# Performance work log

Hardware: AMD Instinct MI355X
Metric: run time of the kernel (lower is better)

The kernel has to match this reference:

```python
import jax, jax.numpy as jnp
import numpy as np

B, C, H, W = 16, 256, 64, 64
NH, HD, NM = 4, 32, 4  # heads, head_dim, memory tokens
HID = NH * HD


def rms_norm(x, g):
    # F.normalize(x, dim=1) * sqrt(C) * g  (channel dim = 1)
    norm = jnp.maximum(jnp.linalg.norm(x, axis=1, keepdims=True), 1e-12)
    return x / norm * (x.shape[1] ** 0.5) * g


def setup_inputs() -> dict:
    key = jax.random.key(0)
    ks = jax.random.split(key, 5)
    return {
        "x": jax.random.normal(ks[0], (B, C, H, W), jnp.float32),
        "g_in": jnp.ones((1, C, 1, 1), jnp.float32),
        "mem_kv": jax.random.normal(ks[1], (2, NH, HD, NM), jnp.float32),
        "w_qkv": jax.random.normal(ks[2], (HID * 3, C), jnp.float32) * (C ** -0.5),
        "w_out": jax.random.normal(ks[3], (C, HID), jnp.float32) * (HID ** -0.5),
        "b_out": jnp.zeros((C,), jnp.float32),
        "g_out": jnp.ones((1, C, 1, 1), jnp.float32),
    }


def reference(x, g_in, mem_kv, w_qkv, w_out, b_out, g_out):
    b, c, h, w = x.shape
    n = h * w
    scale = HD ** -0.5

    xn = rms_norm(x, g_in)
    # 1x1 conv as matmul over channel dim: [B, 3*HID, H, W]
    qkv = jnp.einsum('oc,bchw->bohw', w_qkv, xn)
    q, k, v = jnp.split(qkv, 3, axis=1)
    # b (h d) x y -> b h d n
    q = q.reshape(b, NH, HD, n)
    k = k.reshape(b, NH, HD, n)
    v = v.reshape(b, NH, HD, n)

    # prepend memory key/value tokens: [b, h, d, NM + n]
    mk = jnp.broadcast_to(mem_kv[0], (b, NH, HD, NM))
    mv = jnp.broadcast_to(mem_kv[1], (b, NH, HD, NM))
    k = jnp.concatenate([mk, k], axis=-1)
    v = jnp.concatenate([mv, v], axis=-1)

    q = jax.nn.softmax(q, axis=-2) * scale  # softmax over head_dim
    k = jax.nn.softmax(k, axis=-1)          # softmax over tokens

    context = jnp.einsum('bhdn,bhen->bhde', k, v)  # [b, h, d, e]
    out = jnp.einsum('bhde,bhdn->bhen', context, q)  # [b, h, e, n]
    out = out.reshape(b, HID, h, w)

    out = jnp.einsum('oc,bchw->bohw', w_out, out) + b_out[None, :, None, None]
    return rms_norm(out, g_out)
```

## Files before the change

kernel.cpp:

```cpp
#include <hip/hip_runtime.h>
#include <math.h>

typedef unsigned short u16;
typedef unsigned int u32;

#define NBATCH 16
#define NCH    256
#define NPIX   4096
#define NHEAD  4
#define HDIM   32
#define NMEM   4
#define HID    128
#define OC3    384
#define SCALE_Q 0.17677669529663687f

typedef __bf16 bf16x8 __attribute__((ext_vector_type(8)));
typedef float  f32x4  __attribute__((ext_vector_type(4)));

__device__ __forceinline__ float bf2f(u16 u){ return __uint_as_float(((u32)u)<<16); }
__device__ __forceinline__ u16 f2bf(float f){
  u32 x = __float_as_uint(f);
  x += 0x7fffu + ((x>>16)&1u);
  return (u16)(x>>16);
}
__device__ __forceinline__ void unpack8(int4 v, float* o){
  u32 a=(u32)v.x, b=(u32)v.y, c=(u32)v.z, d=(u32)v.w;
  o[0]=__uint_as_float(a<<16); o[1]=__uint_as_float(a&0xffff0000u);
  o[2]=__uint_as_float(b<<16); o[3]=__uint_as_float(b&0xffff0000u);
  o[4]=__uint_as_float(c<<16); o[5]=__uint_as_float(c&0xffff0000u);
  o[6]=__uint_as_float(d<<16); o[7]=__uint_as_float(d&0xffff0000u);
}
__device__ __forceinline__ void async16(u16* lds, const u16* g){
  __builtin_amdgcn_global_load_lds((const __attribute__((address_space(1))) u32*)g,
                                   (__attribute__((address_space(3))) u32*)lds, 16, 0, 0);
}

__global__ __launch_bounds__(256) void k_pack(const float* __restrict__ wqkv,
                                              const float* __restrict__ gin,
                                              const float* __restrict__ wout,
                                              u16* __restrict__ wqb,
                                              u16* __restrict__ wob)
{
  int i = blockIdx.x*256 + threadIdx.x;
  if (i < OC3*NCH){ int c = i & 255; wqb[i] = f2bf(wqkv[i]*gin[c]); }
  else { int j = i - OC3*NCH; wob[j] = f2bf(wout[j]); }
}

__global__ __launch_bounds__(512) void k_qkvx(const float* __restrict__ x,
                                              const u16* __restrict__ wqb,
                                              u16* __restrict__ qkv)
{
  __shared__ u16 Bx[64*264];
  __shared__ u16 As[384*32];
  __shared__ u16 Ds[128*72];
  __shared__ float ssqp[8][64];
  __shared__ float rl[64];
  const int t = threadIdx.x, w = t>>6, lane = t&63;
  const int n0 = blockIdx.x*64, b = blockIdx.y;
  const int qw = lane>>4, rr = lane&15;

  {
    const float* xp = x + ((size_t)b*NCH + w*32)*NPIX + n0 + lane;
    float ssq = 0.f;
    #pragma unroll
    for (int j=0;j<4;j++){
      u32 pk[4];
      #pragma unroll
      for (int q=0;q<4;q++){
        float v0 = xp[(size_t)(j*8+2*q  )*NPIX];
        float v1 = xp[(size_t)(j*8+2*q+1)*NPIX];
        ssq += v0*v0 + v1*v1;
        pk[q] = (u32)f2bf(v0) | ((u32)f2bf(v1)<<16);
      }
      *(int4*)&Bx[lane*264 + w*32 + j*8] = make_int4((int)pk[0],(int)pk[1],(int)pk[2],(int)pk[3]);
    }
    ssqp[w][lane] = ssq;
  }
  __syncthreads();
  if (t < 64){
    float s = 0.f;
    #pragma unroll
    for (int g=0;g<8;g++) s += ssqp[g][t];
    rl[t] = 16.0f / fmaxf(sqrtf(s), 1e-12f);
  }

  f32x4 acc[3][4];
  #pragma unroll
  for (int p=0;p<3;p++)
    #pragma unroll
    for (int nf=0;nf<4;nf++) acc[p][nf] = (f32x4){0.f,0.f,0.f,0.f};

  for (int c0=0; c0<NCH; c0+=32){
    if (c0) __syncthreads();
    #pragma unroll
    for (int j=0;j<3;j++){
      int rb = w*48 + j*16;
      int row = rb + (lane>>2);
      int gc  = ((lane&3) - (row>>1)) & 3;
      async16(&As[rb*32], wqb + (size_t)row*NCH + c0 + gc*8);
    }
    __syncthreads();
    bf16x8 af[3], bfr[4];
    #pragma unroll
    for (int p=0;p<3;p++){
      int row = p*128 + w*16 + rr;
      int s = (qw + (row>>1)) & 3;
      af[p] = *(const bf16x8*)&As[row*32 + s*8];
    }
    #pragma unroll
    for (int nf=0;nf<4;nf++)
      bfr[nf] = *(const bf16x8*)&Bx[(nf*16+rr)*264 + c0 + qw*8];
    #pragma unroll
    for (int p=0;p<3;p++)
      #pragma unroll
      for (int nf=0;nf<4;nf++)
        acc[p][nf] = __builtin_amdgcn_mfma_f32_16x16x32_bf16(af[p], bfr[nf], acc[p][nf], 0, 0, 0);
  }

  for (int p=0;p<3;p++){
    __syncthreads();
    #pragma unroll
    for (int nf=0;nf<4;nf++){
      int col = nf*16 + rr;
      float rv = rl[col];
      #pragma unroll
      for (int reg=0;reg<4;reg++){
        int rowl = w*16 + qw*4 + reg;
        Ds[rowl*72 + col] = f2bf(acc[p][nf][reg] * rv);
      }
    }
    __syncthreads();
    if (p==0){
      if (t < 256){
        int h = t>>6, n = t&63;
        float v[32];
        float m = -1e30f;
        #pragma unroll
        for (int d=0;d<32;d++){ v[d] = bf2f(Ds[(h*32+d)*72 + n]); m = fmaxf(m, v[d]); }
        float s = 0.f;
        #pragma unroll
        for (int d=0;d<32;d++){ v[d] = __expf(v[d]-m); s += v[d]; }
        float inv = SCALE_Q / s;
        #pragma unroll
        for (int d=0;d<32;d++) Ds[(h*32+d)*72 + n] = f2bf(v[d]*inv);
      }
      __syncthreads();
    }
    int ro = t>>2, seg = (t&3)*16;
    u16* dst = qkv + ((size_t)(b*OC3 + p*128 + ro))*NPIX + n0 + seg;
    *(int4*)dst     = *(const int4*)&Ds[ro*72 + seg];
    *(int4*)(dst+8) = *(const int4*)&Ds[ro*72 + seg + 8];
  }
}

__global__ __launch_bounds__(256) void k_kred(const u16* __restrict__ qkv,
                                              const float* __restrict__ memkv,
                                              float2* __restrict__ kms,
                                              float* __restrict__ ksm)
{
  const int rid = blockIdx.x*4 + (threadIdx.x>>6);
  const int lane = threadIdx.x & 63;
  const int d = rid & 31, h = (rid>>5)&3, b = rid>>7;
  const u16* p = qkv + (size_t)(b*OC3 + HID + h*HDIM + d)*NPIX;
  u32 buf[32];
  #pragma unroll
  for (int j=0;j<8;j++)
    *(int4*)&buf[j*4] = *(const int4*)(p + (size_t)(j*64+lane)*8);
  float m = -1e30f;
  #pragma unroll
  for (int i=0;i<32;i++){
    float lo = __uint_as_float(buf[i]<<16);
    float hi = __uint_as_float(buf[i]&0xffff0000u);
    m = fmaxf(m, fmaxf(lo, hi));
  }
  float mv[4];
  #pragma unroll
  for (int mm=0;mm<4;mm++){ mv[mm] = memkv[(h*HDIM+d)*NMEM + mm]; m = fmaxf(m, mv[mm]); }
  #pragma unroll
  for (int sh=1; sh<64; sh<<=1) m = fmaxf(m, __shfl_xor(m, sh, 64));
  float ssum = 0.f;
  #pragma unroll
  for (int i=0;i<32;i++){
    float lo = __uint_as_float(buf[i]<<16);
    float hi = __uint_as_float(buf[i]&0xffff0000u);
    ssum += __expf(lo-m) + __expf(hi-m);
  }
  #pragma unroll
  for (int sh=1; sh<64; sh<<=1) ssum += __shfl_xor(ssum, sh, 64);
  #pragma unroll
  for (int mm=0;mm<4;mm++) ssum += __expf(mv[mm]-m);
  float inv = 1.0f/ssum;
  if (lane==0) kms[rid] = make_float2(m, inv);
  if (lane<4) ksm[rid*NMEM + lane] = __expf(mv[lane]-m)*inv;
}

__global__ __launch_bounds__(64) void k_ctx(const u16* __restrict__ qkv,
                                            const float* __restrict__ memkv,
                                            const float* __restrict__ ksm,
                                            const float2* __restrict__ kms,
                                            float* __restrict__ ctxp)
{
  __shared__ float Ks[32][132];
  __shared__ float Vs[32][132];
  const int bh = blockIdx.x;
  const int s  = blockIdx.y;
  const int b = bh>>2, h = bh&3;
  const int t = threadIdx.x;
  const int d0 = (t>>3)*4, e0 = (t&7)*4;
  float acc[4][4] = {};
  if (s==0){
    #pragma unroll
    for (int m=0;m<4;m++){
      float km[4];
      #pragma unroll
      for (int pi=0;pi<4;pi++) km[pi] = ksm[(bh*HDIM + d0+pi)*NMEM + m];
      #pragma unroll
      for (int q=0;q<4;q++){
        float vm = memkv[((NHEAD+h)*HDIM + e0+q)*NMEM + m];
        #pragma unroll
        for (int pi=0;pi<4;pi++) acc[pi][q] += km[pi]*vm;
      }
    }
  }
  const u16* kb = qkv + (size_t)(b*OC3 +   HID + h*HDIM)*NPIX;
  const u16* vb = qkv + (size_t)(b*OC3 + 2*HID + h*HDIM)*NPIX;
  const int lr = t>>1, lseg = (t&1)*64;
  const float2 ms = kms[bh*HDIM + lr];
  for (int n0 = s*256; n0 < s*256+256; n0 += 128){
    const u16* kp = kb + (size_t)lr*NPIX + n0 + lseg;
    const u16* vp = vb + (size_t)lr*NPIX + n0 + lseg;
    #pragma unroll
    for (int u=0;u<8;u++){
      int4 kv = *(const int4*)(kp + u*8);
      int4 vv = *(const int4*)(vp + u*8);
      float kf[8], vf[8];
      unpack8(kv,kf); unpack8(vv,vf);
      #pragma unroll
      for (int i=0;i<8;i++) kf[i] = __expf(kf[i]-ms.x)*ms.y;
      *(float4*)&Ks[lr][lseg+u*8]   = make_float4(kf[0],kf[1],kf[2],kf[3]);
      *(float4*)&Ks[lr][lseg+u*8+4] = make_float4(kf[4],kf[5],kf[6],kf[7]);
      *(float4*)&Vs[lr][lseg+u*8]   = make_float4(vf[0],vf[1],vf[2],vf[3]);
      *(float4*)&Vs[lr][lseg+u*8+4] = make_float4(vf[4],vf[5],vf[6],vf[7]);
    }
    __syncthreads();
    #pragma unroll 4
    for (int nn=0;nn<128;nn+=4){
      float kq[4][4] __attribute__((aligned(16)));
      float vq[4][4] __attribute__((aligned(16)));
      #pragma unroll
      for (int pi=0;pi<4;pi++) *(float4*)kq[pi] = *(const float4*)&Ks[d0+pi][nn];
      #pragma unroll
      for (int q=0;q<4;q++)    *(float4*)vq[q]  = *(const float4*)&Vs[e0+q][nn];
      #pragma unroll
      for (int pi=0;pi<4;pi++)
        #pragma unroll
        for (int q=0;q<4;q++)
          acc[pi][q] += kq[pi][0]*vq[q][0] + kq[pi][1]*vq[q][1]
                      + kq[pi][2]*vq[q][2] + kq[pi][3]*vq[q][3];
    }
    __syncthreads();
  }
  #pragma unroll
  for (int pi=0;pi<4;pi++)
    *(float4*)(ctxp + (size_t)(s*64+bh)*1024 + (d0+pi)*32 + e0) =
      make_float4(acc[pi][0],acc[pi][1],acc[pi][2],acc[pi][3]);
}

__global__ __launch_bounds__(256) void k_ctxred(const float* __restrict__ ctxp,
                                                float* __restrict__ ctx)
{
  const int bh = blockIdx.x, t = threadIdx.x;
  float4 s = make_float4(0.f,0.f,0.f,0.f);
  #pragma unroll
  for (int sp=0; sp<16; sp++){
    float4 v = *(const float4*)(ctxp + (size_t)(sp*64+bh)*1024 + t*4);
    s.x+=v.x; s.y+=v.y; s.z+=v.z; s.w+=v.w;
  }
  *(float4*)(ctx + (size_t)bh*1024 + t*4) = s;
}

__global__ __launch_bounds__(256) void k_attnout(const u16* __restrict__ qkv,
                                                 const float* __restrict__ ctx,
                                                 u16* __restrict__ aoT)
{
  const int nc = blockIdx.x, h = blockIdx.y, b = blockIdx.z;
  const int bh = (b<<2) + h;
  const int n = nc*256 + threadIdx.x;
  const float* C = ctx + (size_t)bh*1024;
  const u16* qp = qkv + (size_t)(b*OC3 + h*HDIM)*NPIX + n;
  float qv[32];
  #pragma unroll
  for (int d=0;d<32;d++) qv[d] = bf2f(qp[(size_t)d*NPIX]);
  float res[32];
  #pragma unroll
  for (int eb=0;eb<8;eb++){
    float s0=0.f,s1=0.f,s2=0.f,s3=0.f;
    #pragma unroll
    for (int d=0;d<32;d++){
      float4 cv = *(const float4*)(C + d*32 + eb*4);
      float qd = qv[d];
      s0 += cv.x*qd; s1 += cv.y*qd; s2 += cv.z*qd; s3 += cv.w*qd;
    }
    res[eb*4+0]=s0; res[eb*4+1]=s1; res[eb*4+2]=s2; res[eb*4+3]=s3;
  }
  u16* op = aoT + ((size_t)b*NPIX + n)*HID + h*HDIM;
  #pragma unroll
  for (int i=0;i<4;i++){
    u32 pk[4];
    #pragma unroll
    for (int q=0;q<4;q++)
      pk[q] = (u32)f2bf(res[i*8+2*q]) | ((u32)f2bf(res[i*8+2*q+1])<<16);
    *(int4*)(op + i*8) = make_int4((int)pk[0],(int)pk[1],(int)pk[2],(int)pk[3]);
  }
}

__global__ __launch_bounds__(256) void k_out(const u16* __restrict__ wob,
                                             const u16* __restrict__ aoT,
                                             const float* __restrict__ bout,
                                             const float* __restrict__ gout,
                                             float* __restrict__ out)
{
  __shared__ u16 As[256*32];
  __shared__ u16 Bs[64*32];
  __shared__ float ssql[4][64];
  const int t = threadIdx.x, w = t>>6, lane = t&63;
  const int n0 = blockIdx.x*64, b = blockIdx.y;
  const int qw = lane>>4, rr = lane&15;
  f32x4 acc[4][4];
  #pragma unroll
  for (int i=0;i<4;i++)
    #pragma unroll
    for (int j=0;j<4;j++) acc[i][j] = (f32x4){0.f,0.f,0.f,0.f};

  const u16* Bg = aoT + ((size_t)b*NPIX + n0)*HID;

  for (int k0=0; k0<HID; k0+=32){
    if (k0) __syncthreads();
    #pragma unroll
    for (int j=0;j<4;j++){
      int rb = w*64 + j*16;
      int row = rb + (lane>>2);
      int gc  = ((lane&3) - (row>>1)) & 3;
      async16(&As[rb*32], wob + (size_t)row*HID + k0 + gc*8);
    }
    {
      int rb = w*16;
      int row = rb + (lane>>2);
      int gc  = ((lane&3) - (row>>1)) & 3;
      async16(&Bs[rb*32], Bg + (size_t)row*HID + k0 + gc*8);
    }
    __syncthreads();
    bf16x8 af[4], bfr[4];
    #pragma unroll
    for (int mf=0;mf<4;mf++){
      int row = w*64 + mf*16 + rr;
      int s = (qw + (row>>1)) & 3;
      af[mf] = *(const bf16x8*)&As[row*32 + s*8];
    }
    #pragma unroll
    for (int nf=0;nf<4;nf++){
      int row = nf*16 + rr;
      int s = (qw + (row>>1)) & 3;
      bfr[nf] = *(const bf16x8*)&Bs[row*32 + s*8];
    }
    #pragma unroll
    for (int mf=0;mf<4;mf++)
      #pragma unroll
      for (int nf=0;nf<4;nf++)
        acc[mf][nf] = __builtin_amdgcn_mfma_f32_16x16x32_bf16(af[mf], bfr[nf], acc[mf][nf], 0, 0, 0);
  }
  __syncthreads();
  float pssq[4] = {0.f,0.f,0.f,0.f};
  #pragma unroll
  for (int mf=0;mf<4;mf++)
    #pragma unroll
    for (int reg=0;reg<4;reg++){
      int c = w*64 + mf*16 + qw*4 + reg;
      float bb = bout[c];
      #pragma unroll
      for (int nf=0;nf<4;nf++){
        float v = acc[mf][nf][reg] + bb;
        acc[mf][nf][reg] = v;
        pssq[nf] += v*v;
      }
    }
  #pragma unroll
  for (int nf=0;nf<4;nf++){
    pssq[nf] += __shfl_xor(pssq[nf], 16, 64);
    pssq[nf] += __shfl_xor(pssq[nf], 32, 64);
  }
  if (qw==0){
    #pragma unroll
    for (int nf=0;nf<4;nf++) ssql[w][nf*16+rr] = pssq[nf];
  }
  __syncthreads();
  float rv[4];
  #pragma unroll
  for (int nf=0;nf<4;nf++){
    int col = nf*16 + rr;
    float sm = ssql[0][col]+ssql[1][col]+ssql[2][col]+ssql[3][col];
    rv[nf] = 16.0f / fmaxf(sqrtf(sm), 1e-12f);
  }
  #pragma unroll
  for (int mf=0;mf<4;mf++)
    #pragma unroll
    for (int reg=0;reg<4;reg++){
      int c = w*64 + mf*16 + qw*4 + reg;
      float g = gout[c];
      float* po = out + ((size_t)(b*NCH + c))*NPIX + n0;
      #pragma unroll
      for (int nf=0;nf<4;nf++)
        po[nf*16 + rr] = acc[mf][nf][reg]*rv[nf]*g;
    }
}

extern "C" void kernel_launch(void* const* d_in, const int* in_sizes, int n_in,
                              void* d_out, int out_size, void* d_ws, size_t ws_size,
                              hipStream_t stream)
{
  const float* x     = (const float*)d_in[0];
  const float* gin   = (const float*)d_in[1];
  const float* memkv = (const float*)d_in[2];
  const float* wqkv  = (const float*)d_in[3];
  const float* wout  = (const float*)d_in[4];
  const float* bout  = (const float*)d_in[5];
  const float* gout  = (const float*)d_in[6];
  float* out = (float*)d_out;

  char* ws = (char*)d_ws;
  u16*    qkv  = (u16*)   (ws);
  float*  ksm  = (float*) (ws + 50331648);
  float2* kms  = (float2*)(ws + 50364416);
  float*  ctxp = (float*) (ws + 50380800);
  float*  ctx  = (float*) (ws + 54575104);
  u16*    aoT  = (u16*)   (ws + 54837248);
  u16*    wqb  = (u16*)   (ws + 71614464);
  u16*    wob  = (u16*)   (ws + 71811072);

  hipLaunchKernelGGL(k_pack,   dim3(512),     dim3(256), 0, stream, wqkv, gin, wout, wqb, wob);
  hipLaunchKernelGGL(k_qkvx,   dim3(64,16),   dim3(512), 0, stream, x, wqb, qkv);
  hipLaunchKernelGGL(k_kred,   dim3(512),     dim3(256), 0, stream, qkv, memkv, kms, ksm);
  hipLaunchKernelGGL(k_ctx,    dim3(64,16),   dim3(64),  0, stream, qkv, memkv, ksm, kms, ctxp);
  hipLaunchKernelGGL(k_ctxred, dim3(64),      dim3(256), 0, stream, ctxp, ctx);
  hipLaunchKernelGGL(k_attnout,dim3(16,4,16), dim3(256), 0, stream, qkv, ctx, aoT);
  hipLaunchKernelGGL(k_out,    dim3(64,16),   dim3(256), 0, stream, wob, aoT, bout, gout, out);
}
```

Before: 211.7 us.

## Fuse attention-output and projection kernels, read weights directly, split context wider

Merges k_attnout into the output projection kernel. Per-pixel context application now runs as MFMA from LDS tiles of Q and a bf16 context, so the intermediate aoT buffer is never written to or read from global memory. The QKV and output GEMMs load weight fragments straight from global memory instead of staging them through LDS with async loads, which removes per-k-step barriers and frees LDS. The context kernel gets twice as many blocks, each covering 128 tokens, and the reduction sums 32 partials. The tradeoffs are more uncoalesced global weight loads and bf16 rounding of the context.

```diff
diff --git a/kernel.cpp b/kernel.cpp
--- a/kernel.cpp
+++ b/kernel.cpp
@@ -30,10 +30,6 @@
   o[4]=__uint_as_float(c<<16); o[5]=__uint_as_float(c&0xffff0000u);
   o[6]=__uint_as_float(d<<16); o[7]=__uint_as_float(d&0xffff0000u);
 }
-__device__ __forceinline__ void async16(u16* lds, const u16* g){
-  __builtin_amdgcn_global_load_lds((const __attribute__((address_space(1))) u32*)g,
-                                   (__attribute__((address_space(3))) u32*)lds, 16, 0, 0);
-}
 
 __global__ __launch_bounds__(256) void k_pack(const float* __restrict__ wqkv,
                                               const float* __restrict__ gin,
@@ -50,11 +46,10 @@
                                               const u16* __restrict__ wqb,
                                               u16* __restrict__ qkv)
 {
-  __shared__ u16 Bx[64*264];
-  __shared__ u16 As[384*32];
-  __shared__ u16 Ds[128*72];
+  __shared__ u16 BxDs[64*264];
   __shared__ float ssqp[8][64];
   __shared__ float rl[64];
+  u16* Ds = BxDs;
   const int t = threadIdx.x, w = t>>6, lane = t&63;
   const int n0 = blockIdx.x*64, b = blockIdx.y;
   const int qw = lane>>4, rr = lane&15;
@@ -72,7 +67,7 @@
         ssq += v0*v0 + v1*v1;
         pk[q] = (u32)f2bf(v0) | ((u32)f2bf(v1)<<16);
       }
-      *(int4*)&Bx[lane*264 + w*32 + j*8] = make_int4((int)pk[0],(int)pk[1],(int)pk[2],(int)pk[3]);
+      *(int4*)&BxDs[lane*264 + w*32 + j*8] = make_int4((int)pk[0],(int)pk[1],(int)pk[2],(int)pk[3]);
     }
     ssqp[w][lane] = ssq;
   }
@@ -90,31 +85,24 @@
     #pragma unroll
     for (int nf=0;nf<4;nf++) acc[p][nf] = (f32x4){0.f,0.f,0.f,0.f};
 
+  const u16* a0 = wqb + (size_t)(0*128 + w*16 + rr)*NCH + qw*8;
+  const u16* a1 = wqb + (size_t)(1*128 + w*16 + rr)*NCH + qw*8;
+  const u16* a2 = wqb + (size_t)(2*128 + w*16 + rr)*NCH + qw*8;
+  #pragma unroll
   for (int c0=0; c0<NCH; c0+=32){
-    if (c0) __syncthreads();
-    #pragma unroll
-    for (int j=0;j<3;j++){
-      int rb = w*48 + j*16;
-      int row = rb + (lane>>2);
-      int gc  = ((lane&3) - (row>>1)) & 3;
-      async16(&As[rb*32], wqb + (size_t)row*NCH + c0 + gc*8);
-    }
-    __syncthreads();
-    bf16x8 af[3], bfr[4];
-    #pragma unroll
-    for (int p=0;p<3;p++){
-      int row = p*128 + w*16 + rr;
-      int s = (qw + (row>>1)) & 3;
-      af[p] = *(const bf16x8*)&As[row*32 + s*8];
-    }
+    bf16x8 af0 = *(const bf16x8*)(a0 + c0);
+    bf16x8 af1 = *(const bf16x8*)(a1 + c0);
+    bf16x8 af2 = *(const bf16x8*)(a2 + c0);
+    bf16x8 bfr[4];
     #pragma unroll
     for (int nf=0;nf<4;nf++)
-      bfr[nf] = *(const bf16x8*)&Bx[(nf*16+rr)*264 + c0 + qw*8];
-    #pragma unroll
-    for (int p=0;p<3;p++)
-      #pragma unroll
-      for (int nf=0;nf<4;nf++)
-        acc[p][nf] = __builtin_amdgcn_mfma_f32_16x16x32_bf16(af[p], bfr[nf], acc[p][nf], 0, 0, 0);
+      bfr[nf] = *(const bf16x8*)&BxDs[(nf*16+rr)*264 + c0 + qw*8];
+    #pragma unroll
+    for (int nf=0;nf<4;nf++){
+      acc[0][nf] = __builtin_amdgcn_mfma_f32_16x16x32_bf16(af0, bfr[nf], acc[0][nf], 0, 0, 0);
+      acc[1][nf] = __builtin_amdgcn_mfma_f32_16x16x32_bf16(af1, bfr[nf], acc[1][nf], 0, 0, 0);
+      acc[2][nf] = __builtin_amdgcn_mfma_f32_16x16x32_bf16(af2, bfr[nf], acc[2][nf], 0, 0, 0);
+    }
   }
 
   for (int p=0;p<3;p++){
@@ -226,7 +214,8 @@
   const u16* vb = qkv + (size_t)(b*OC3 + 2*HID + h*HDIM)*NPIX;
   const int lr = t>>1, lseg = (t&1)*64;
   const float2 ms = kms[bh*HDIM + lr];
-  for (int n0 = s*256; n0 < s*256+256; n0 += 128){
+  const int n0 = s*128;
+  {
     const u16* kp = kb + (size_t)lr*NPIX + n0 + lseg;
     const u16* vp = vb + (size_t)lr*NPIX + n0 + lseg;
     #pragma unroll
@@ -258,7 +247,6 @@
           acc[pi][q] += kq[pi][0]*vq[q][0] + kq[pi][1]*vq[q][1]
                       + kq[pi][2]*vq[q][2] + kq[pi][3]*vq[q][3];
     }
-    __syncthreads();
   }
   #pragma unroll
   for (int pi=0;pi<4;pi++)
@@ -272,104 +260,94 @@
   const int bh = blockIdx.x, t = threadIdx.x;
   float4 s = make_float4(0.f,0.f,0.f,0.f);
   #pragma unroll
-  for (int sp=0; sp<16; sp++){
+  for (int sp=0; sp<32; sp++){
     float4 v = *(const float4*)(ctxp + (size_t)(sp*64+bh)*1024 + t*4);
     s.x+=v.x; s.y+=v.y; s.z+=v.z; s.w+=v.w;
   }
   *(float4*)(ctx + (size_t)bh*1024 + t*4) = s;
 }
 
-__global__ __launch_bounds__(256) void k_attnout(const u16* __restrict__ qkv,
-                                                 const float* __restrict__ ctx,
-                                                 u16* __restrict__ aoT)
-{
-  const int nc = blockIdx.x, h = blockIdx.y, b = blockIdx.z;
-  const int bh = (b<<2) + h;
-  const int n = nc*256 + threadIdx.x;
-  const float* C = ctx + (size_t)bh*1024;
-  const u16* qp = qkv + (size_t)(b*OC3 + h*HDIM)*NPIX + n;
-  float qv[32];
-  #pragma unroll
-  for (int d=0;d<32;d++) qv[d] = bf2f(qp[(size_t)d*NPIX]);
-  float res[32];
-  #pragma unroll
-  for (int eb=0;eb<8;eb++){
-    float s0=0.f,s1=0.f,s2=0.f,s3=0.f;
-    #pragma unroll
-    for (int d=0;d<32;d++){
-      float4 cv = *(const float4*)(C + d*32 + eb*4);
-      float qd = qv[d];
-      s0 += cv.x*qd; s1 += cv.y*qd; s2 += cv.z*qd; s3 += cv.w*qd;
-    }
-    res[eb*4+0]=s0; res[eb*4+1]=s1; res[eb*4+2]=s2; res[eb*4+3]=s3;
-  }
-  u16* op = aoT + ((size_t)b*NPIX + n)*HID + h*HDIM;
-  #pragma unroll
-  for (int i=0;i<4;i++){
-    u32 pk[4];
-    #pragma unroll
-    for (int q=0;q<4;q++)
-      pk[q] = (u32)f2bf(res[i*8+2*q]) | ((u32)f2bf(res[i*8+2*q+1])<<16);
-    *(int4*)(op + i*8) = make_int4((int)pk[0],(int)pk[1],(int)pk[2],(int)pk[3]);
-  }
-}
-
-__global__ __launch_bounds__(256) void k_out(const u16* __restrict__ wob,
-                                             const u16* __restrict__ aoT,
-                                             const float* __restrict__ bout,
-                                             const float* __restrict__ gout,
-                                             float* __restrict__ out)
-{
-  __shared__ u16 As[256*32];
-  __shared__ u16 Bs[64*32];
+__global__ __launch_bounds__(256) void k_fout(const u16* __restrict__ qkv,
+                                              const float* __restrict__ ctx,
+                                              const u16* __restrict__ wob,
+                                              const float* __restrict__ bout,
+                                              const float* __restrict__ gout,
+                                              float* __restrict__ out)
+{
+  __shared__ u16 Cb[4*32*40];
+  __shared__ u16 Qs[64*136];
+  __shared__ u16 Ao[64*136];
   __shared__ float ssql[4][64];
   const int t = threadIdx.x, w = t>>6, lane = t&63;
   const int n0 = blockIdx.x*64, b = blockIdx.y;
   const int qw = lane>>4, rr = lane&15;
+
+  {
+    const float4* c4 = (const float4*)(ctx + (size_t)b*4096);
+    const int d = (t>>3)&31, e0 = (t&7)*4;
+    #pragma unroll
+    for (int h=0;h<4;h++){
+      float4 v = c4[t + h*256];
+      Cb[(h*32+e0+0)*40 + d] = f2bf(v.x);
+      Cb[(h*32+e0+1)*40 + d] = f2bf(v.y);
+      Cb[(h*32+e0+2)*40 + d] = f2bf(v.z);
+      Cb[(h*32+e0+3)*40 + d] = f2bf(v.w);
+    }
+  }
+  {
+    const int ro = t>>1, nh = (t&1)*32;
+    const u16* qp = qkv + ((size_t)(b*OC3 + ro))*NPIX + n0 + nh;
+    u16 tmp[32];
+    *(int4*)&tmp[0]  = *(const int4*)(qp);
+    *(int4*)&tmp[8]  = *(const int4*)(qp+8);
+    *(int4*)&tmp[16] = *(const int4*)(qp+16);
+    *(int4*)&tmp[24] = *(const int4*)(qp+24);
+    #pragma unroll
+    for (int j=0;j<32;j++) Qs[(nh+j)*136 + ro] = tmp[j];
+  }
+  __syncthreads();
+
+  f32x4 pv[4][2];
+  #pragma unroll
+  for (int h=0;h<4;h++){
+    bf16x8 bq = *(const bf16x8*)&Qs[(w*16+rr)*136 + h*32 + qw*8];
+    #pragma unroll
+    for (int ef=0;ef<2;ef++){
+      bf16x8 af = *(const bf16x8*)&Cb[(h*32 + ef*16 + rr)*40 + qw*8];
+      f32x4 z = (f32x4){0.f,0.f,0.f,0.f};
+      pv[h][ef] = __builtin_amdgcn_mfma_f32_16x16x32_bf16(af, bq, z, 0, 0, 0);
+    }
+  }
+  #pragma unroll
+  for (int h=0;h<4;h++)
+    #pragma unroll
+    for (int ef=0;ef<2;ef++){
+      u32 lohi0 = (u32)f2bf(pv[h][ef][0]) | ((u32)f2bf(pv[h][ef][1])<<16);
+      u32 lohi1 = (u32)f2bf(pv[h][ef][2]) | ((u32)f2bf(pv[h][ef][3])<<16);
+      *(int2*)&Ao[(w*16+rr)*136 + h*32 + ef*16 + qw*4] = make_int2((int)lohi0,(int)lohi1);
+    }
+  __syncthreads();
+
   f32x4 acc[4][4];
   #pragma unroll
   for (int i=0;i<4;i++)
     #pragma unroll
     for (int j=0;j<4;j++) acc[i][j] = (f32x4){0.f,0.f,0.f,0.f};
-
-  const u16* Bg = aoT + ((size_t)b*NPIX + n0)*HID;
-
+  #pragma unroll
   for (int k0=0; k0<HID; k0+=32){
-    if (k0) __syncthreads();
-    #pragma unroll
-    for (int j=0;j<4;j++){
-      int rb = w*64 + j*16;
-      int row = rb + (lane>>2);
-      int gc  = ((lane&3) - (row>>1)) & 3;
-      async16(&As[rb*32], wob + (size_t)row*HID + k0 + gc*8);
-    }
-    {
-      int rb = w*16;
-      int row = rb + (lane>>2);
-      int gc  = ((lane&3) - (row>>1)) & 3;
-      async16(&Bs[rb*32], Bg + (size_t)row*HID + k0 + gc*8);
-    }
-    __syncthreads();
     bf16x8 af[4], bfr[4];
     #pragma unroll
-    for (int mf=0;mf<4;mf++){
-      int row = w*64 + mf*16 + rr;
-      int s = (qw + (row>>1)) & 3;
-      af[mf] = *(const bf16x8*)&As[row*32 + s*8];
-    }
-    #pragma unroll
-    for (int nf=0;nf<4;nf++){
-      int row = nf*16 + rr;
-      int s = (qw + (row>>1)) & 3;
-      bfr[nf] = *(const bf16x8*)&Bs[row*32 + s*8];
-    }
+    for (int mf=0;mf<4;mf++)
+      af[mf] = *(const bf16x8*)&wob[(size_t)(w*64 + mf*16 + rr)*HID + k0 + qw*8];
+    #pragma unroll
+    for (int nf=0;nf<4;nf++)
+      bfr[nf] = *(const bf16x8*)&Ao[(nf*16+rr)*136 + k0 + qw*8];
     #pragma unroll
     for (int mf=0;mf<4;mf++)
       #pragma unroll
       for (int nf=0;nf<4;nf++)
         acc[mf][nf] = __builtin_amdgcn_mfma_f32_16x16x32_bf16(af[mf], bfr[nf], acc[mf][nf], 0, 0, 0);
   }
-  __syncthreads();
   float pssq[4] = {0.f,0.f,0.f,0.f};
   #pragma unroll
   for (int mf=0;mf<4;mf++)
@@ -432,16 +410,14 @@
   float*  ksm  = (float*) (ws + 50331648);
   float2* kms  = (float2*)(ws + 50364416);
   float*  ctxp = (float*) (ws + 50380800);
-  float*  ctx  = (float*) (ws + 54575104);
-  u16*    aoT  = (u16*)   (ws + 54837248);
-  u16*    wqb  = (u16*)   (ws + 71614464);
-  u16*    wob  = (u16*)   (ws + 71811072);
-
-  hipLaunchKernelGGL(k_pack,   dim3(512),     dim3(256), 0, stream, wqkv, gin, wout, wqb, wob);
-  hipLaunchKernelGGL(k_qkvx,   dim3(64,16),   dim3(512), 0, stream, x, wqb, qkv);
-  hipLaunchKernelGGL(k_kred,   dim3(512),     dim3(256), 0, stream, qkv, memkv, kms, ksm);
-  hipLaunchKernelGGL(k_ctx,    dim3(64,16),   dim3(64),  0, stream, qkv, memkv, ksm, kms, ctxp);
-  hipLaunchKernelGGL(k_ctxred, dim3(64),      dim3(256), 0, stream, ctxp, ctx);
-  hipLaunchKernelGGL(k_attnout,dim3(16,4,16), dim3(256), 0, stream, qkv, ctx, aoT);
-  hipLaunchKernelGGL(k_out,    dim3(64,16),   dim3(256), 0, stream, wob, aoT, bout, gout, out);
-}
+  float*  ctx  = (float*) (ws + 58769408);
+  u16*    wqb  = (u16*)   (ws + 59031552);
+  u16*    wob  = (u16*)   (ws + 59228160);
+
+  hipLaunchKernelGGL(k_pack,   dim3(512),   dim3(256), 0, stream, wqkv, gin, wout, wqb, wob);
+  hipLaunchKernelGGL(k_qkvx,   dim3(64,16), dim3(512), 0, stream, x, wqb, qkv);
+  hipLaunchKernelGGL(k_kred,   dim3(512),   dim3(256), 0, stream, qkv, memkv, kms, ksm);
+  hipLaunchKernelGGL(k_ctx,    dim3(64,32), dim3(64),  0, stream, qkv, memkv, ksm, kms, ctxp);
+  hipLaunchKernelGGL(k_ctxred, dim3(64),    dim3(256), 0, stream, ctxp, ctx);
+  hipLaunchKernelGGL(k_fout,   dim3(64,16), dim3(256), 0, stream, qkv, ctx, wob, bout, gout, out);
+}
```

Result: faster. 200.4 us (-5.4%).
